# Performance work log

Hardware: AMD Instinct MI355X
Metric: run time of the kernel (lower is better)

Reference implementation:

```python
import jax, jax.numpy as jnp
import numpy as np
import math

B, MSA, L, D = 1, 64, 256, 512
H = 8
DH = D // H  # 64


def setup_inputs() -> dict:
    key = jax.random.key(0)
    ks = jax.random.split(key, 6)
    x = jax.random.normal(ks[0], (B, MSA, L, D), dtype=jnp.float32)
    Wq = jax.random.normal(ks[1], (D, D), dtype=jnp.float32) * (1.0 / math.sqrt(D))
    Wk = jax.random.normal(ks[2], (D, D), dtype=jnp.float32) * (1.0 / math.sqrt(D))
    Wv = jax.random.normal(ks[3], (D, D), dtype=jnp.float32) * (1.0 / math.sqrt(D))
    aK = jax.random.normal(ks[4], (L, L, DH), dtype=jnp.float32)
    aV = jax.random.normal(ks[5], (L, L, DH), dtype=jnp.float32)
    return {"x": x, "Wq": Wq, "Wk": Wk, "Wv": Wv, "aK": aK, "aV": aV}


def _proj(t, W, b, m, l, h, dh):
    # nn.Linear(bias=False): t @ W.T, then split heads -> (B,H,MSA,L,dh)
    y = jnp.einsum('bmld,ed->bmle', t, W).reshape(b, m, l, h, dh)
    return jnp.transpose(y, (0, 3, 1, 2, 4))


def reference(x, Wq, Wk, Wv, aK, aV):
    b, m, l, d = x.shape
    h, dh = H, DH
    q = _proj(x, Wq, b, m, l, h, dh)  # (B,H,MSA,L,dh)
    k = _proj(x, Wk, b, m, l, h, dh)
    v = _proj(x, Wv, b, m, l, h, dh)
    # content score + relative-position score
    e1 = jnp.einsum('bhmid,bhmjd->bhmij', q, k)           # (B,H,MSA,L,L)
    e2 = jnp.einsum('bhmid,ijd->bhmij', q, aK)            # (B,H,MSA,L,L)
    alpha = jax.nn.softmax((e1 + e2) / math.sqrt(dh), axis=-1)
    z1 = jnp.einsum('bhmij,bhmjd->bhmid', alpha, v)       # content output
    z2 = jnp.einsum('bhmij,ijd->bhmid', alpha, aV)        # relative-V output
    z = (z1 + z2).sum(axis=2)                             # sum over MSA -> (B,H,L,dh)
    out = jnp.transpose(z, (0, 2, 1, 3)).reshape(b, l, d) # (B,L,D)
    return out
```

## Files before the change

### kernel.cpp

```cpp
#include <hip/hip_runtime.h>

#define THREADS 256

typedef unsigned short u16;
typedef __attribute__((ext_vector_type(8))) short bf16x8;
typedef __attribute__((ext_vector_type(4))) float f32x4;

__device__ __forceinline__ u16 f2bf(float f) {
  unsigned int u = __float_as_uint(f);
  u += 0x7fffu + ((u >> 16) & 1u);
  return (u16)(u >> 16);
}
__device__ __forceinline__ float bf2f(u16 s) {
  return __uint_as_float(((unsigned int)s) << 16);
}
__device__ __forceinline__ bf16x8 ld8g(const u16* p) {
  return *reinterpret_cast<const bf16x8*>(p);
}
__device__ __forceinline__ bf16x8 ld8s(const u16* p) {
  return *reinterpret_cast<const bf16x8*>(p);
}
__device__ __forceinline__ void st4bf(u16* dst, float4 v) {
  unsigned int lo = (unsigned int)f2bf(v.x) | ((unsigned int)f2bf(v.y) << 16);
  unsigned int hi = (unsigned int)f2bf(v.z) | ((unsigned int)f2bf(v.w) << 16);
  uint2 u; u.x = lo; u.y = hi;
  *reinterpret_cast<uint2*>(dst) = u;
}
__device__ __forceinline__ uint4 pack8(float4 a, float4 b) {
  uint4 r;
  r.x = (unsigned int)f2bf(a.x) | ((unsigned int)f2bf(a.y) << 16);
  r.y = (unsigned int)f2bf(a.z) | ((unsigned int)f2bf(a.w) << 16);
  r.z = (unsigned int)f2bf(b.x) | ((unsigned int)f2bf(b.y) << 16);
  r.w = (unsigned int)f2bf(b.z) | ((unsigned int)f2bf(b.w) << 16);
  return r;
}
typedef __attribute__((address_space(1))) const unsigned int g_u32;
typedef __attribute__((address_space(3))) unsigned int l_u32;
__device__ __forceinline__ void async16(const u16* g, u16* l) {
  __builtin_amdgcn_global_load_lds((g_u32*)g, (l_u32*)l, 16, 0, 0);
}

__global__ __launch_bounds__(THREADS) void cast_xw(
    const float* __restrict__ x, const float* __restrict__ wq,
    const float* __restrict__ wk, const float* __restrict__ wv,
    u16* __restrict__ xb, u16* __restrict__ wqb, u16* __restrict__ wkb,
    u16* __restrict__ wvb) {
  int t = blockIdx.x * THREADS + threadIdx.x;
  if (t < 2097152) {
    st4bf(xb + t * 4, reinterpret_cast<const float4*>(x)[t]);
  } else if (t < 2162688) {
    int q = t - 2097152;
    st4bf(wqb + q * 4, reinterpret_cast<const float4*>(wq)[q]);
  } else if (t < 2228224) {
    int q = t - 2162688;
    st4bf(wkb + q * 4, reinterpret_cast<const float4*>(wk)[q]);
  } else if (t < 2293760) {
    int q = t - 2228224;
    st4bf(wvb + q * 4, reinterpret_cast<const float4*>(wv)[q]);
  }
}

__global__ __launch_bounds__(THREADS) void proj_gemm(
    const u16* __restrict__ xb, const u16* __restrict__ wb,
    u16* __restrict__ qh, u16* __restrict__ kb, u16* __restrict__ vt) {
  const int bm = blockIdx.x / 12, bn = blockIdx.x % 12;
  const int tid = threadIdx.x;
  const int wave = tid >> 6, lane = tid & 63;
  const int quad = lane >> 4, l15 = lane & 15;
  __shared__ __align__(16) u16 smem[9216];
  u16* At = smem;
  u16* Bt = smem + 4096;

  const int rowL = lane >> 2;
  const int chunkL = (lane & 3) ^ ((lane >> 3) & 3);
  const u16* gA = xb + (size_t)(bm * 128 + wave * 32 + rowL) * 512 + chunkL * 8;
  const u16* gB = wb + (size_t)(bn * 128 + wave * 32 + rowL) * 512 + chunkL * 8;
  u16* lA = At + wave * 1024;
  u16* lB = Bt + wave * 1024;

  const int rw0 = (wave & 1) * 64, cw0 = (wave >> 1) * 64;
  const int swz = (quad ^ ((l15 >> 1) & 3)) * 8;

  f32x4 acc[4][4];
#pragma unroll
  for (int mt = 0; mt < 4; ++mt)
#pragma unroll
    for (int nt = 0; nt < 4; ++nt) acc[mt][nt] = (f32x4){0.f, 0.f, 0.f, 0.f};

  for (int s = 0; s < 16; ++s) {
    __syncthreads();
    async16(gA + s * 32, lA);
    async16(gA + s * 32 + 8192, lA + 512);
    async16(gB + s * 32, lB);
    async16(gB + s * 32 + 8192, lB + 512);
    __syncthreads();
    bf16x8 af[4], bf[4];
#pragma unroll
    for (int mt = 0; mt < 4; ++mt)
      af[mt] = ld8s(At + (rw0 + mt * 16 + l15) * 32 + swz);
#pragma unroll
    for (int nt = 0; nt < 4; ++nt)
      bf[nt] = ld8s(Bt + (cw0 + nt * 16 + l15) * 32 + swz);
#pragma unroll
    for (int mt = 0; mt < 4; ++mt)
#pragma unroll
      for (int nt = 0; nt < 4; ++nt)
        acc[mt][nt] = __builtin_amdgcn_mfma_f32_16x16x32_bf16(af[mt], bf[nt], acc[mt][nt], 0, 0, 0);
  }

  const int mat = bn >> 2;
  const int h0 = (bn & 3) * 2;
  const int m = bm >> 1;
  const int l0 = (bm & 1) * 128;

  if (mat < 2) {
    u16* dstb = (mat == 0) ? qh : kb;
    const int il = tid >> 1, cc = (tid & 1) * 32;
#pragma unroll
    for (int p = 0; p < 2; ++p) {
      __syncthreads();
      if ((wave >> 1) == p) {
#pragma unroll
        for (int mt = 0; mt < 4; ++mt)
#pragma unroll
          for (int nt = 0; nt < 4; ++nt)
#pragma unroll
            for (int r = 0; r < 4; ++r)
              smem[(rw0 + mt * 16 + quad * 4 + r) * 72 + nt * 16 + l15] =
                  f2bf(acc[mt][nt][r]);
      }
      __syncthreads();
      u16* dst = dstb + ((size_t)((h0 + p) * 64 + m) * 256 + l0 + il) * 64 + cc;
      uint4 v0 = *reinterpret_cast<uint4*>(&smem[il * 72 + cc]);
      uint4 v1 = *reinterpret_cast<uint4*>(&smem[il * 72 + cc + 8]);
      uint4 v2 = *reinterpret_cast<uint4*>(&smem[il * 72 + cc + 16]);
      uint4 v3 = *reinterpret_cast<uint4*>(&smem[il * 72 + cc + 24]);
      *reinterpret_cast<uint4*>(dst) = v0;
      *reinterpret_cast<uint4*>(dst + 8) = v1;
      *reinterpret_cast<uint4*>(dst + 16) = v2;
      *reinterpret_cast<uint4*>(dst + 24) = v3;
    }
  } else {
    const int tl = tid >> 2, cc = (tid & 3) * 32;
#pragma unroll
    for (int p = 0; p < 2; ++p) {
      __syncthreads();
      if ((wave >> 1) == p) {
#pragma unroll
        for (int mt = 0; mt < 4; ++mt)
#pragma unroll
          for (int nt = 0; nt < 4; ++nt)
#pragma unroll
            for (int r = 0; r < 4; ++r)
              smem[(nt * 16 + l15) * 136 + rw0 + mt * 16 + quad * 4 + r] =
                  f2bf(acc[mt][nt][r]);
      }
      __syncthreads();
      int hm = (h0 + p) * 64 + m;
      u16* dst = vt + (size_t)hm * 16384 + tl * 256 + l0 + cc;
      uint4 v0 = *reinterpret_cast<uint4*>(&smem[tl * 136 + cc]);
      uint4 v1 = *reinterpret_cast<uint4*>(&smem[tl * 136 + cc + 8]);
      uint4 v2 = *reinterpret_cast<uint4*>(&smem[tl * 136 + cc + 16]);
      uint4 v3 = *reinterpret_cast<uint4*>(&smem[tl * 136 + cc + 24]);
      *reinterpret_cast<uint4*>(dst) = v0;
      *reinterpret_cast<uint4*>(dst + 8) = v1;
      *reinterpret_cast<uint4*>(dst + 16) = v2;
      *reinterpret_cast<uint4*>(dst + 24) = v3;
    }
  }
}

__global__ __launch_bounds__(THREADS) void e2_k(
    const u16* __restrict__ qh, const float* __restrict__ aK,
    u16* __restrict__ e2g) {
  const int i = blockIdx.x >> 3, hmt = blockIdx.x & 7;
  const int tid = threadIdx.x;
  const int wave = tid >> 6, lane = tid & 63;
  const int quad = lane >> 4, l15 = lane & 15;
  __shared__ u16 aKl[256 * 72];
#pragma unroll
  for (int c = 0; c < 8; ++c) {
    int fidx = c * 2048 + tid * 8;
    int j = fidx >> 6, d = fidx & 63;
    float4 f0 = *reinterpret_cast<const float4*>(aK + i * 16384 + fidx);
    float4 f1 = *reinterpret_cast<const float4*>(aK + i * 16384 + fidx + 4);
    *reinterpret_cast<uint4*>(&aKl[j * 72 + d]) = pack8(f0, f1);
  }
  __syncthreads();
  f32x4 acc[16];
#pragma unroll
  for (int nt = 0; nt < 16; ++nt) acc[nt] = (f32x4){0.f, 0.f, 0.f, 0.f};
  bf16x8 a[2];
#pragma unroll
  for (int ks = 0; ks < 2; ++ks)
    a[ks] = ld8g(qh + ((hmt * 64 + wave * 16 + l15) * 256 + i) * 64 + ks * 32 + quad * 8);
#pragma unroll
  for (int nt = 0; nt < 16; ++nt) {
#pragma unroll
    for (int ks = 0; ks < 2; ++ks) {
      bf16x8 b = ld8s(&aKl[(nt * 16 + l15) * 72 + ks * 32 + quad * 8]);
      acc[nt] = __builtin_amdgcn_mfma_f32_16x16x32_bf16(a[ks], b, acc[nt], 0, 0, 0);
    }
  }
  __syncthreads();
  u16* S = aKl;
#pragma unroll
  for (int nt = 0; nt < 16; ++nt)
#pragma unroll
    for (int r = 0; r < 4; ++r)
      S[(wave * 16 + quad * 4 + r) * 264 + nt * 16 + l15] = f2bf(acc[nt][r]);
  __syncthreads();
#pragma unroll
  for (int c = 0; c < 8; ++c) {
    int lin = c * 2048 + tid * 8;
    int row = lin >> 8, col = lin & 255;
    uint4 v = *reinterpret_cast<uint4*>(&S[row * 264 + col]);
    *reinterpret_cast<uint4*>(e2g + ((size_t)(hmt * 64 + row) * 256 + i) * 256 + col) = v;
  }
}

__global__ __launch_bounds__(THREADS, 2) void attn_f(
    const u16* __restrict__ qh, const u16* __restrict__ kb,
    const u16* __restrict__ vt, u16* __restrict__ e2g,
    u16* __restrict__ z1q) {
  const int bi = blockIdx.x;
  const int it = bi >> 8;
  const int hmc = bi & 255;
  const int h = hmc >> 5, mc = hmc & 31;
  const int tid = threadIdx.x;
  const int wave = tid >> 6, lane = tid & 63;
  const int quad = lane >> 4, l15 = lane & 15;
  __shared__ u16 As[4 * 4224];
  u16* W = &As[wave * 4224];
  const int i0 = it * 64 + wave * 16;

  f32x4 betaacc[16];
  f32x4 acc2[4];
#pragma unroll
  for (int nt = 0; nt < 16; ++nt) betaacc[nt] = (f32x4){0.f, 0.f, 0.f, 0.f};
#pragma unroll
  for (int nt = 0; nt < 4; ++nt) acc2[nt] = (f32x4){0.f, 0.f, 0.f, 0.f};

  for (int mi = 0; mi < 2; ++mi) {
    const int hm = h * 64 + mc * 2 + mi;
    {
      const u16* e2p = e2g + ((size_t)hm * 256 + i0) * 256;
#pragma unroll
      for (int c = 0; c < 8; ++c) {
        int lin = c * 512 + lane * 8;
        int row = lin >> 8, col = lin & 255;
        uint4 v = *reinterpret_cast<const uint4*>(e2p + row * 256 + col);
        *reinterpret_cast<uint4*>(&W[row * 264 + col]) = v;
      }
    }
    f32x4 acc[16];
#pragma unroll
    for (int nt = 0; nt < 16; ++nt)
#pragma unroll
      for (int r = 0; r < 4; ++r)
        acc[nt][r] = bf2f(W[(quad * 4 + r) * 264 + nt * 16 + l15]);
    bf16x8 a[2];
#pragma unroll
    for (int ks = 0; ks < 2; ++ks)
      a[ks] = ld8g(qh + ((size_t)hm * 256 + i0 + l15) * 64 + ks * 32 + quad * 8);
#pragma unroll
    for (int nt = 0; nt < 16; ++nt) {
#pragma unroll
      for (int ks = 0; ks < 2; ++ks) {
        bf16x8 b = ld8g(kb + ((size_t)hm * 256 + nt * 16 + l15) * 64 + ks * 32 + quad * 8);
        acc[nt] = __builtin_amdgcn_mfma_f32_16x16x32_bf16(a[ks], b, acc[nt], 0, 0, 0);
      }
    }
#pragma unroll
    for (int r = 0; r < 4; ++r) {
      float mx = -3.0e38f;
#pragma unroll
      for (int nt = 0; nt < 16; ++nt) mx = fmaxf(mx, acc[nt][r]);
      for (int msk = 1; msk < 16; msk <<= 1) mx = fmaxf(mx, __shfl_xor(mx, msk));
      float s = 0.f;
#pragma unroll
      for (int nt = 0; nt < 16; ++nt) {
        float p = expf((acc[nt][r] - mx) * 0.125f);
        acc[nt][r] = p;
        s += p;
      }
      for (int msk = 1; msk < 16; msk <<= 1) s += __shfl_xor(s, msk);
      float inv = 1.0f / s;
      int lrow = quad * 4 + r;
#pragma unroll
      for (int nt = 0; nt < 16; ++nt) {
        float av = acc[nt][r] * inv;
        betaacc[nt][r] += av;
        W[lrow * 264 + nt * 16 + l15] = f2bf(av);
      }
    }
#pragma unroll
    for (int ks = 0; ks < 8; ++ks) {
      bf16x8 a2 = ld8s(&W[l15 * 264 + ks * 32 + quad * 8]);
#pragma unroll
      for (int nt = 0; nt < 4; ++nt) {
        bf16x8 b2 = ld8g(vt + (size_t)hm * 16384 + (nt * 16 + l15) * 256 + ks * 32 + quad * 8);
        acc2[nt] = __builtin_amdgcn_mfma_f32_16x16x32_bf16(a2, b2, acc2[nt], 0, 0, 0);
      }
    }
  }

#pragma unroll
  for (int nt = 0; nt < 16; ++nt)
#pragma unroll
    for (int r = 0; r < 4; ++r)
      W[(quad * 4 + r) * 264 + nt * 16 + l15] = f2bf(betaacc[nt][r]);
#pragma unroll
  for (int c = 0; c < 8; ++c) {
    int lin = c * 512 + lane * 8;
    int row = lin >> 8, col = lin & 255;
    uint4 v = *reinterpret_cast<uint4*>(&W[row * 264 + col]);
    *reinterpret_cast<uint4*>(
        e2g + ((size_t)(h * 64 + mc * 2) * 256 + it * 64 + wave * 16 + row) * 256 + col) = v;
  }
#pragma unroll
  for (int nt = 0; nt < 4; ++nt)
#pragma unroll
    for (int r = 0; r < 4; ++r)
      W[(quad * 4 + r) * 72 + nt * 16 + l15] = f2bf(acc2[nt][r]);
  {
    int row = lane >> 2, col = (lane & 3) * 16;
    uint4 v0 = *reinterpret_cast<uint4*>(&W[row * 72 + col]);
    uint4 v1 = *reinterpret_cast<uint4*>(&W[row * 72 + col + 8]);
    u16* dst = z1q + ((size_t)(h * 32 + mc) * 256 + it * 64 + wave * 16 + row) * 64 + col;
    *reinterpret_cast<uint4*>(dst) = v0;
    *reinterpret_cast<uint4*>(dst + 8) = v1;
  }
}

__global__ __launch_bounds__(THREADS) void beta_r(
    const u16* __restrict__ betap, float* __restrict__ beta) {
  int t = blockIdx.x * THREADS + threadIdx.x;
  int hi = t >> 5;
  int j0 = (t & 31) * 8;
  int h = hi >> 8, i = hi & 255;
  const u16* src = betap + (size_t)(h * 64) * 65536 + i * 256 + j0;
  float s[8] = {0.f, 0.f, 0.f, 0.f, 0.f, 0.f, 0.f, 0.f};
#pragma unroll
  for (int m = 0; m < 32; ++m) {
    uint4 v = *reinterpret_cast<const uint4*>(src + (size_t)m * 131072);
    const u16* pv = reinterpret_cast<const u16*>(&v);
#pragma unroll
    for (int u = 0; u < 8; ++u) s[u] += bf2f(pv[u]);
  }
  float4 o0 = {s[0], s[1], s[2], s[3]};
  float4 o1 = {s[4], s[5], s[6], s[7]};
  *reinterpret_cast<float4*>(beta + (size_t)hi * 256 + j0) = o0;
  *reinterpret_cast<float4*>(beta + (size_t)hi * 256 + j0 + 4) = o1;
}

__global__ __launch_bounds__(THREADS) void z2_k(
    const float* __restrict__ beta, const float* __restrict__ aV,
    float* __restrict__ z2b) {
  const int i = blockIdx.x;
  const int tid = threadIdx.x;
  const int wave = tid >> 6, lane = tid & 63;
  const int quad = lane >> 4, l15 = lane & 15;
  __shared__ u16 aVl[64 * 264];
#pragma unroll
  for (int c = 0; c < 8; ++c) {
    int fidx = c * 2048 + tid * 8;
    int j = fidx >> 6, d = fidx & 63;
    float4 f0 = *reinterpret_cast<const float4*>(aV + (size_t)i * 16384 + fidx);
    float4 f1 = *reinterpret_cast<const float4*>(aV + (size_t)i * 16384 + fidx + 4);
    float fv[8] = {f0.x, f0.y, f0.z, f0.w, f1.x, f1.y, f1.z, f1.w};
#pragma unroll
    for (int u = 0; u < 8; ++u) aVl[(d + u) * 264 + j] = f2bf(fv[u]);
  }
  __syncthreads();
  f32x4 acc = (f32x4){0.f, 0.f, 0.f, 0.f};
#pragma unroll
  for (int ks = 0; ks < 8; ++ks) {
    u16 ab[8];
    if (l15 < 8) {
      const float* bp = beta + (l15 * 256 + i) * 256 + ks * 32 + quad * 8;
      float4 f0 = *reinterpret_cast<const float4*>(bp);
      float4 f1 = *reinterpret_cast<const float4*>(bp + 4);
      ab[0] = f2bf(f0.x); ab[1] = f2bf(f0.y); ab[2] = f2bf(f0.z); ab[3] = f2bf(f0.w);
      ab[4] = f2bf(f1.x); ab[5] = f2bf(f1.y); ab[6] = f2bf(f1.z); ab[7] = f2bf(f1.w);
    } else {
#pragma unroll
      for (int u = 0; u < 8; ++u) ab[u] = 0;
    }
    bf16x8 a = *reinterpret_cast<bf16x8*>(ab);
    bf16x8 b = ld8s(&aVl[(wave * 16 + l15) * 264 + ks * 32 + quad * 8]);
    acc = __builtin_amdgcn_mfma_f32_16x16x32_bf16(a, b, acc, 0, 0, 0);
  }
#pragma unroll
  for (int r = 0; r < 4; ++r) {
    int hh = quad * 4 + r;
    if (hh < 8) z2b[i * 512 + hh * 64 + wave * 16 + l15] = acc[r];
  }
}

__global__ __launch_bounds__(THREADS) void final_k(
    const u16* __restrict__ z1q, const float* __restrict__ z2b,
    float* __restrict__ out) {
  int o = blockIdx.x * THREADS + threadIdx.x;
  int i = o >> 9, e = o & 511;
  int h = e >> 6, d = e & 63;
  float s = z2b[o];
  const u16* base = z1q + ((size_t)(h * 32) * 256 + i) * 64 + d;
#pragma unroll
  for (int m = 0; m < 32; ++m) s += bf2f(base[(size_t)m * 16384]);
  out[o] = s;
}

extern "C" void kernel_launch(void* const* d_in, const int* in_sizes, int n_in,
                              void* d_out, int out_size, void* d_ws, size_t ws_size,
                              hipStream_t stream) {
  const float* x  = (const float*)d_in[0];
  const float* wq = (const float*)d_in[1];
  const float* wk = (const float*)d_in[2];
  const float* wv = (const float*)d_in[3];
  const float* aK = (const float*)d_in[4];
  const float* aV = (const float*)d_in[5];
  float* out = (float*)d_out;

  char* ws = (char*)d_ws;
  u16* xb    = (u16*)(ws + 0);
  u16* wqb   = (u16*)(ws + 16777216);
  u16* wkb   = (u16*)(ws + 17301504);
  u16* wvb   = (u16*)(ws + 17825792);
  u16* qh    = (u16*)(ws + 35127296);
  u16* kb    = (u16*)(ws + 51904512);
  u16* vt    = (u16*)(ws + 68681728);
  u16* e2g   = (u16*)(ws + 85458944);
  u16* z1q   = xb;
  float* beta= (float*)(ws + 8388608);
  float* z2b = (float*)(ws + 10485760);

  cast_xw<<<8960, THREADS, 0, stream>>>(x, wq, wk, wv, xb, wqb, wkb, wvb);
  proj_gemm<<<1536, THREADS, 0, stream>>>(xb, wqb, qh, kb, vt);
  e2_k<<<2048, THREADS, 0, stream>>>(qh, aK, e2g);
  attn_f<<<1024, THREADS, 0, stream>>>(qh, kb, vt, e2g, z1q);
  beta_r<<<256, THREADS, 0, stream>>>(e2g, beta);
  z2_k<<<256, THREADS, 0, stream>>>(beta, aV, z2b);
  final_k<<<512, THREADS, 0, stream>>>(z1q, z2b, out);
}
```

Measured before the change: 304.5 us.

## Stage q in LDS for e2, use fp16 beta accumulators, raise attn occupancy

```diff
diff --git a/kernel.cpp b/kernel.cpp
--- a/kernel.cpp
+++ b/kernel.cpp
@@ -3,8 +3,10 @@
 #define THREADS 256
 
 typedef unsigned short u16;
+typedef _Float16 f16;
 typedef __attribute__((ext_vector_type(8))) short bf16x8;
 typedef __attribute__((ext_vector_type(4))) float f32x4;
+typedef __attribute__((ext_vector_type(4))) _Float16 f16x4;
 
 __device__ __forceinline__ u16 f2bf(float f) {
   unsigned int u = __float_as_uint(f);
@@ -13,6 +15,12 @@
 }
 __device__ __forceinline__ float bf2f(u16 s) {
   return __uint_as_float(((unsigned int)s) << 16);
+}
+__device__ __forceinline__ u16 f16bits(f16 v) {
+  union { f16 h; u16 u; } c; c.h = v; return c.u;
+}
+__device__ __forceinline__ float f16tof(u16 b) {
+  union { u16 u; f16 h; } c; c.u = b; return (float)c.h;
 }
 __device__ __forceinline__ bf16x8 ld8g(const u16* p) {
   return *reinterpret_cast<const bf16x8*>(p);
@@ -173,11 +181,12 @@
 __global__ __launch_bounds__(THREADS) void e2_k(
     const u16* __restrict__ qh, const float* __restrict__ aK,
     u16* __restrict__ e2g) {
-  const int i = blockIdx.x >> 3, hmt = blockIdx.x & 7;
+  const int hmt = blockIdx.x >> 8, i = blockIdx.x & 255;
   const int tid = threadIdx.x;
   const int wave = tid >> 6, lane = tid & 63;
   const int quad = lane >> 4, l15 = lane & 15;
   __shared__ u16 aKl[256 * 72];
+  __shared__ u16 qL[64 * 72];
 #pragma unroll
   for (int c = 0; c < 8; ++c) {
     int fidx = c * 2048 + tid * 8;
@@ -186,6 +195,14 @@
     float4 f1 = *reinterpret_cast<const float4*>(aK + i * 16384 + fidx + 4);
     *reinterpret_cast<uint4*>(&aKl[j * 72 + d]) = pack8(f0, f1);
   }
+#pragma unroll
+  for (int c = 0; c < 4; ++c) {
+    int r = c * 16 + (tid >> 4);
+    int dd = (tid & 15) * 4;
+    uint2 v = *reinterpret_cast<const uint2*>(
+        qh + ((size_t)(hmt * 64 + r) * 256 + i) * 64 + dd);
+    *reinterpret_cast<uint2*>(&qL[r * 72 + dd]) = v;
+  }
   __syncthreads();
   f32x4 acc[16];
 #pragma unroll
@@ -193,7 +210,7 @@
   bf16x8 a[2];
 #pragma unroll
   for (int ks = 0; ks < 2; ++ks)
-    a[ks] = ld8g(qh + ((hmt * 64 + wave * 16 + l15) * 256 + i) * 64 + ks * 32 + quad * 8);
+    a[ks] = ld8s(&qL[(wave * 16 + l15) * 72 + ks * 32 + quad * 8]);
 #pragma unroll
   for (int nt = 0; nt < 16; ++nt) {
 #pragma unroll
@@ -219,7 +236,7 @@
   }
 }
 
-__global__ __launch_bounds__(THREADS, 2) void attn_f(
+__global__ __launch_bounds__(THREADS, 3) void attn_f(
     const u16* __restrict__ qh, const u16* __restrict__ kb,
     const u16* __restrict__ vt, u16* __restrict__ e2g,
     u16* __restrict__ z1q) {
@@ -234,10 +251,10 @@
   u16* W = &As[wave * 4224];
   const int i0 = it * 64 + wave * 16;
 
-  f32x4 betaacc[16];
+  f16x4 betaacc[16];
   f32x4 acc2[4];
 #pragma unroll
-  for (int nt = 0; nt < 16; ++nt) betaacc[nt] = (f32x4){0.f, 0.f, 0.f, 0.f};
+  for (int nt = 0; nt < 16; ++nt) betaacc[nt] = (f16x4){0, 0, 0, 0};
 #pragma unroll
   for (int nt = 0; nt < 4; ++nt) acc2[nt] = (f32x4){0.f, 0.f, 0.f, 0.f};
 
@@ -280,7 +297,7 @@
       float s = 0.f;
 #pragma unroll
       for (int nt = 0; nt < 16; ++nt) {
-        float p = expf((acc[nt][r] - mx) * 0.125f);
+        float p = __expf((acc[nt][r] - mx) * 0.125f);
         acc[nt][r] = p;
         s += p;
       }
@@ -290,7 +307,7 @@
 #pragma unroll
       for (int nt = 0; nt < 16; ++nt) {
         float av = acc[nt][r] * inv;
-        betaacc[nt][r] += av;
+        betaacc[nt][r] += (f16)av;
         W[lrow * 264 + nt * 16 + l15] = f2bf(av);
       }
     }
@@ -309,7 +326,7 @@
   for (int nt = 0; nt < 16; ++nt)
 #pragma unroll
     for (int r = 0; r < 4; ++r)
-      W[(quad * 4 + r) * 264 + nt * 16 + l15] = f2bf(betaacc[nt][r]);
+      W[(quad * 4 + r) * 264 + nt * 16 + l15] = f16bits(betaacc[nt][r]);
 #pragma unroll
   for (int c = 0; c < 8; ++c) {
     int lin = c * 512 + lane * 8;
@@ -346,7 +363,7 @@
     uint4 v = *reinterpret_cast<const uint4*>(src + (size_t)m * 131072);
     const u16* pv = reinterpret_cast<const u16*>(&v);
 #pragma unroll
-    for (int u = 0; u < 8; ++u) s[u] += bf2f(pv[u]);
+    for (int u = 0; u < 8; ++u) s[u] += f16tof(pv[u]);
   }
   float4 o0 = {s[0], s[1], s[2], s[3]};
   float4 o1 = {s[4], s[5], s[6], s[7]};
```

After: 318.4 us. 4.6% more time.
